# Kernel optimization log

Hardware: AMD Instinct MI355X
Metric: run time of the kernel (lower is better)

The kernel has to match this reference:

```python
import jax, jax.numpy as jnp
import numpy as np

N_NODES = 100000
N_EDGES = 1600000
IN_DIM = 128
HID = 128
OUT = 40


def setup_inputs() -> dict:
    key = jax.random.key(0)
    ks = jax.random.split(key, 8)
    x = jax.random.normal(ks[0], (N_NODES, IN_DIM), dtype=jnp.float32)
    edge_index = jax.random.randint(ks[1], (2, N_EDGES), 0, N_NODES, dtype=jnp.int64)
    def glorot(k, fan_in, fan_out):
        s = jnp.sqrt(6.0 / (fan_in + fan_out)).astype(jnp.float32)
        return jax.random.uniform(k, (fan_in, fan_out), jnp.float32, -s, s)
    return {
        "x": x,
        "edge_index": edge_index,
        "W1": glorot(ks[2], IN_DIM, HID), "b1": jnp.zeros((HID,), jnp.float32),
        "W2": glorot(ks[3], HID, HID),    "b2": jnp.zeros((HID,), jnp.float32),
        "W3": glorot(ks[4], HID, HID),    "b3": jnp.zeros((HID,), jnp.float32),
        "Wl": glorot(ks[5], HID, OUT),    "bl": jnp.zeros((OUT,), jnp.float32),
    }


def _gcn_norm(edge_index, num_nodes):
    # PyG GCNConv default: add self-loops, symmetric normalization.
    loops = jnp.arange(num_nodes, dtype=edge_index.dtype)
    src = jnp.concatenate([edge_index[0], loops])
    dst = jnp.concatenate([edge_index[1], loops])
    deg = jax.ops.segment_sum(jnp.ones_like(dst, dtype=jnp.float32), dst,
                              num_segments=num_nodes)
    dis = jnp.where(deg > 0, jax.lax.rsqrt(deg), 0.0)  # deg^{-1/2}
    norm = dis[src] * dis[dst]  # [E+N]
    return src, dst, norm


def _gcn_conv(x, W, b, src, dst, norm, num_nodes):
    h = x @ W                                   # [N, F_out]
    msg = h[src] * norm[:, None]                # gather + scale
    out = jax.ops.segment_sum(msg, dst, num_segments=num_nodes)
    return out + b


def reference(x, edge_index, W1, b1, W2, b2, W3, b3, Wl, bl):
    n = x.shape[0]
    src, dst, norm = _gcn_norm(edge_index, n)
    h = jax.nn.relu(_gcn_conv(x, W1, b1, src, dst, norm, n))
    h = jax.nn.relu(_gcn_conv(h, W2, b2, src, dst, norm, n))
    h = _gcn_conv(h, W3, b3, src, dst, norm, n)
    # dropout p=0.5 is identity in eval mode
    return h @ Wl + bl
```

## Files before the change

### kernel.cpp

```cpp
#include <hip/hip_runtime.h>

typedef __attribute__((ext_vector_type(8))) short sh8;
typedef __attribute__((ext_vector_type(4))) float f4;

__device__ __forceinline__ float bf2f(unsigned short u) {
    union { unsigned int u; float f; } c; c.u = ((unsigned int)u) << 16; return c.f;
}
__device__ __forceinline__ unsigned short f2bf(float f) {
    union { float f; unsigned int u; } c; c.f = f;
    unsigned int x = c.u;
    unsigned int r = (x + 0x7fffu + ((x >> 16) & 1u)) >> 16;
    return (unsigned short)r;
}
__device__ __forceinline__ void bfsplit(float x, short& hi, short& lo) {
    unsigned short h = f2bf(x);
    float r = x - bf2f(h);
    hi = (short)h;
    lo = (short)f2bf(r);
}

#define CG_BLOCKS 1024
#define CG_COUNT  512
#define CSR_GRID  1568

__global__ void k_init(int* cnt8, int M,
                       const float* __restrict__ W1, unsigned short* __restrict__ sp) {
    int j = blockIdx.x * 256 + threadIdx.x;
    if (j < M) cnt8[j] = 0;
    if (j < 16384) {
        int k = j >> 7, col = j & 127;
        int t = col * 128 + k;
        short h, l;
        bfsplit(W1[j], h, l);
        sp[t] = (unsigned short)h;
        sp[16384 + t] = (unsigned short)l;
    }
}

__device__ __forceinline__ void count_body(const int* __restrict__ dst,
                                           int* __restrict__ cnt8,
                                           int* __restrict__ rank, int E, int N) {
    int cidx = blockIdx.x >> 1;
    int base = (cidx & 7) * N;
    int E4 = E >> 2;
    for (int i = cidx * 256 + threadIdx.x; i < E4; i += CG_COUNT * 256) {
        int4 d = ((const int4*)dst)[i];
        int4 r;
        r.x = ((unsigned)d.x < (unsigned)N) ? atomicAdd(&cnt8[base + d.x], 1) : -1;
        r.y = ((unsigned)d.y < (unsigned)N) ? atomicAdd(&cnt8[base + d.y], 1) : -1;
        r.z = ((unsigned)d.z < (unsigned)N) ? atomicAdd(&cnt8[base + d.z], 1) : -1;
        r.w = ((unsigned)d.w < (unsigned)N) ? atomicAdd(&cnt8[base + d.w], 1) : -1;
        ((int4*)rank)[i] = r;
    }
    if (cidx == 0) {
        for (int e = (E4 << 2) + threadIdx.x; e < E; e += 256) {
            int d = dst[e];
            rank[e] = ((unsigned)d < (unsigned)N) ? atomicAdd(&cnt8[d], 1) : -1;
        }
    }
}

__device__ __forceinline__ void gemm1_body(const float* __restrict__ X,
                                           const unsigned short* __restrict__ Wh,
                                           const unsigned short* __restrict__ Wl,
                                           unsigned short* __restrict__ H, int nPairs) {
    int gidx = blockIdx.x >> 1;
    int wave = threadIdx.x >> 6;
    int lane = threadIdx.x & 63;
    int ln = lane & 15, quad = lane >> 4;
    int c0 = (wave & 1) * 64;
    int subTile = wave >> 1;

    for (int p = gidx; p < nPairs; p += CG_COUNT) {
        int nodeBase = p * 32 + subTile * 16;
        const float* xrow = X + (nodeBase + ln) * 128 + quad * 8;
        sh8 ah[4], al[4];
        #pragma unroll
        for (int kt = 0; kt < 4; ++kt) {
            f4 v0 = *(const f4*)(xrow + kt * 32);
            f4 v1 = *(const f4*)(xrow + kt * 32 + 4);
            #pragma unroll
            for (int j = 0; j < 4; ++j) {
                short h, l;
                bfsplit(v0[j], h, l); ah[kt][j] = h; al[kt][j] = l;
                bfsplit(v1[j], h, l); ah[kt][j + 4] = h; al[kt][j + 4] = l;
            }
        }

        f4 acc[4] = { {0.f,0.f,0.f,0.f}, {0.f,0.f,0.f,0.f}, {0.f,0.f,0.f,0.f}, {0.f,0.f,0.f,0.f} };
        #pragma unroll
        for (int kt = 0; kt < 4; ++kt) {
            int k0 = kt * 32 + quad * 8;
            #pragma unroll
            for (int nt = 0; nt < 4; ++nt) {
                int col = c0 + nt * 16 + ln;
                sh8 bh = *(const sh8*)(Wh + col * 128 + k0);
                sh8 bl = *(const sh8*)(Wl + col * 128 + k0);
                acc[nt] = __builtin_amdgcn_mfma_f32_16x16x32_bf16(ah[kt], bh, acc[nt], 0, 0, 0);
                acc[nt] = __builtin_amdgcn_mfma_f32_16x16x32_bf16(ah[kt], bl, acc[nt], 0, 0, 0);
                acc[nt] = __builtin_amdgcn_mfma_f32_16x16x32_bf16(al[kt], bh, acc[nt], 0, 0, 0);
            }
        }

        #pragma unroll
        for (int nt = 0; nt < 4; ++nt) {
            int col = c0 + nt * 16 + ln;
            #pragma unroll
            for (int r = 0; r < 4; ++r)
                H[(nodeBase + quad * 4 + r) * 128 + col] = f2bf(acc[nt][r]);
        }
    }
}

__global__ __launch_bounds__(256)
void k_count_gemm1(const int* __restrict__ dst, int* __restrict__ cnt8,
                   int* __restrict__ rank, int E, int N,
                   const float* __restrict__ X,
                   const unsigned short* __restrict__ Wh,
                   const unsigned short* __restrict__ Wl,
                   unsigned short* __restrict__ H, int nPairs) {
    if ((blockIdx.x & 1) == 0)
        count_body(dst, cnt8, rank, E, N);
    else
        gemm1_body(X, Wh, Wl, H, nPairs);
}

#define SCAN_B 256
__global__ void k_scan_a(const int* __restrict__ cnt8, int* __restrict__ rowptr,
                         int* __restrict__ off8, int* __restrict__ deg,
                         int* __restrict__ bsum, float* __restrict__ dis, int N) {
    __shared__ int sh[SCAN_B];
    int t = threadIdx.x, i = blockIdx.x * SCAN_B + t;
    int c[8];
    int v = 0;
    if (i < N) {
        #pragma unroll
        for (int g = 0; g < 8; ++g) { c[g] = cnt8[g * N + i]; v += c[g]; }
        dis[i] = rsqrtf((float)(v + 1));
        deg[i] = v;
    }
    sh[t] = v; __syncthreads();
    for (int off = 1; off < SCAN_B; off <<= 1) {
        int x = (t >= off) ? sh[t - off] : 0;
        __syncthreads();
        sh[t] += x;
        __syncthreads();
    }
    int incl = sh[t];
    if (i < N) {
        int b = incl - v;
        rowptr[i] = b;
        int o = b;
        #pragma unroll
        for (int g = 0; g < 8; ++g) { off8[g * N + i] = o; o += c[g]; }
    }
    if (t == SCAN_B - 1) bsum[blockIdx.x] = incl;
}

__global__ void k_scan_b(int* bsum, int NB) {
    __shared__ int sh[512];
    int t = threadIdx.x;
    int v = (t < NB) ? bsum[t] : 0;
    sh[t] = v; __syncthreads();
    for (int off = 1; off < 512; off <<= 1) {
        int x = (t >= off) ? sh[t - off] : 0;
        __syncthreads();
        sh[t] += x;
        __syncthreads();
    }
    if (t < NB) bsum[t] = sh[t] - v;
}

__global__ void k_scan_c(int* __restrict__ rowptr, int* __restrict__ off8,
                         const int* __restrict__ bsum, int N) {
    int i = blockIdx.x * 256 + threadIdx.x;
    if (i < N) {
        int b = bsum[blockIdx.x];
        rowptr[i] += b;
        #pragma unroll
        for (int g = 0; g < 8; ++g) off8[g * N + i] += b;
    }
}

__global__ void k_fill(const int* __restrict__ src, const int* __restrict__ dst,
                       const int* __restrict__ rank, const int* __restrict__ off8,
                       int* __restrict__ csrc, int E, int N) {
    int E4 = E >> 2;
    for (int i = blockIdx.x * 256 + threadIdx.x; i < E4; i += gridDim.x * 256) {
        int g = (i >> 8) & 7;
        const int* off = off8 + g * N;
        int4 d4 = ((const int4*)dst)[i];
        int4 s4 = ((const int4*)src)[i];
        int4 r4 = ((const int4*)rank)[i];
        #pragma unroll
        for (int q = 0; q < 4; ++q) {
            int d = (q == 0) ? d4.x : (q == 1) ? d4.y : (q == 2) ? d4.z : d4.w;
            int s = (q == 0) ? s4.x : (q == 1) ? s4.y : (q == 2) ? s4.z : s4.w;
            int r = (q == 0) ? r4.x : (q == 1) ? r4.y : (q == 2) ? r4.z : r4.w;
            if ((unsigned)d >= (unsigned)N || (unsigned)s >= (unsigned)N || r < 0) continue;
            csrc[off[d] + r] = s;
        }
    }
    if (blockIdx.x == 0) {
        for (int e = (E4 << 2) + threadIdx.x; e < E; e += 256) {
            int d = dst[e];
            int s = src[e];
            int r = rank[e];
            if ((unsigned)d >= (unsigned)N || (unsigned)s >= (unsigned)N || r < 0) continue;
            csrc[off8[d] + r] = s;
        }
    }
}

__global__ __launch_bounds__(256)
void k_gemm128_a16(const unsigned short* __restrict__ X,
                   const float* __restrict__ W,
                   const float* __restrict__ dis,
                   unsigned short* __restrict__ H, int nPairs) {
    int wave = threadIdx.x >> 6;
    int lane = threadIdx.x & 63;
    int ln = lane & 15, quad = lane >> 4;
    int c0 = (wave & 1) * 64;
    int subTile = wave >> 1;

    sh8 bh[4][4], blo[4][4];
    #pragma unroll
    for (int nt = 0; nt < 4; ++nt) {
        int col = c0 + nt * 16 + ln;
        #pragma unroll
        for (int kt = 0; kt < 4; ++kt) {
            int k0 = kt * 32 + quad * 8;
            #pragma unroll
            for (int j = 0; j < 8; ++j) {
                short h, l;
                bfsplit(W[(k0 + j) * 128 + col], h, l);
                bh[nt][kt][j] = h; blo[nt][kt][j] = l;
            }
        }
    }

    int p = blockIdx.x;
    sh8 a[4];
    if (p < nPairs) {
        const unsigned short* xrow = X + ((size_t)(p * 32 + subTile * 16 + ln)) * 128 + quad * 8;
        #pragma unroll
        for (int kt = 0; kt < 4; ++kt) a[kt] = *(const sh8*)(xrow + kt * 32);
    }
    while (p < nPairs) {
        int pn = p + (int)gridDim.x;
        sh8 an[4];
        if (pn < nPairs) {
            const unsigned short* xn = X + ((size_t)(pn * 32 + subTile * 16 + ln)) * 128 + quad * 8;
            #pragma unroll
            for (int kt = 0; kt < 4; ++kt) an[kt] = *(const sh8*)(xn + kt * 32);
        }

        f4 acc[4] = { {0.f,0.f,0.f,0.f}, {0.f,0.f,0.f,0.f}, {0.f,0.f,0.f,0.f}, {0.f,0.f,0.f,0.f} };
        #pragma unroll
        for (int kt = 0; kt < 4; ++kt)
            #pragma unroll
            for (int nt = 0; nt < 4; ++nt) {
                acc[nt] = __builtin_amdgcn_mfma_f32_16x16x32_bf16(a[kt], bh[nt][kt], acc[nt], 0, 0, 0);
                acc[nt] = __builtin_amdgcn_mfma_f32_16x16x32_bf16(a[kt], blo[nt][kt], acc[nt], 0, 0, 0);
            }

        int nodeBase = p * 32 + subTile * 16;
        float ds[4];
        #pragma unroll
        for (int r = 0; r < 4; ++r) ds[r] = dis[nodeBase + quad * 4 + r];
        #pragma unroll
        for (int nt = 0; nt < 4; ++nt) {
            int col = c0 + nt * 16 + ln;
            #pragma unroll
            for (int r = 0; r < 4; ++r)
                H[(nodeBase + quad * 4 + r) * 128 + col] = f2bf(acc[nt][r] * ds[r]);
        }

        #pragma unroll
        for (int kt = 0; kt < 4; ++kt) a[kt] = an[kt];
        p = pn;
    }
}

__global__ __launch_bounds__(256)
void k_agg(const unsigned short* __restrict__ H,
           unsigned short* __restrict__ O,
           const float* __restrict__ dis,
           const int* __restrict__ rowptr,
           const int* __restrict__ deg,
           const int* __restrict__ csrc,
           const float* __restrict__ bias,
           int relu, int scaled, int N) {
    int n = (blockIdx.x * 256 + threadIdx.x) >> 5;
    if (n >= N) return;
    int lane = threadIdx.x & 31;
    int sub  = lane & 15;
    int half = lane >> 4;

    float a0 = 0.f, a1 = 0.f, a2 = 0.f, a3 = 0.f;
    float a4 = 0.f, a5 = 0.f, a6 = 0.f, a7 = 0.f;
    float dn = dis[n];

    auto addrow = [&](uint4 v) {
        a0 += bf2f((unsigned short)v.x);
        a1 += bf2f((unsigned short)(v.x >> 16));
        a2 += bf2f((unsigned short)v.y);
        a3 += bf2f((unsigned short)(v.y >> 16));
        a4 += bf2f((unsigned short)v.z);
        a5 += bf2f((unsigned short)(v.z >> 16));
        a6 += bf2f((unsigned short)v.w);
        a7 += bf2f((unsigned short)(v.w >> 16));
    };
    auto addroww = [&](uint4 v, float w) {
        a0 = fmaf(w, bf2f((unsigned short)v.x), a0);
        a1 = fmaf(w, bf2f((unsigned short)(v.x >> 16)), a1);
        a2 = fmaf(w, bf2f((unsigned short)v.y), a2);
        a3 = fmaf(w, bf2f((unsigned short)(v.y >> 16)), a3);
        a4 = fmaf(w, bf2f((unsigned short)v.z), a4);
        a5 = fmaf(w, bf2f((unsigned short)(v.z >> 16)), a5);
        a6 = fmaf(w, bf2f((unsigned short)v.w), a6);
        a7 = fmaf(w, bf2f((unsigned short)(v.w >> 16)), a7);
    };

    if (half == 0) {
        uint4 v = *(const uint4*)(H + (size_t)n * 128 + sub * 8);
        if (scaled) addrow(v); else addroww(v, dn);
    }

    int start = rowptr[n];
    int e = deg[n];
    int i = 0;
    if (scaled) {
        for (; i + 8 <= e; i += 8) {
            int s[4];
            #pragma unroll
            for (int q = 0; q < 4; ++q) s[q] = csrc[start + i + 2 * q + half];
            uint4 v[4];
            #pragma unroll
            for (int q = 0; q < 4; ++q) v[q] = *(const uint4*)(H + (size_t)s[q] * 128 + sub * 8);
            #pragma unroll
            for (int q = 0; q < 4; ++q) addrow(v[q]);
        }
        for (int j = i + half; j < e; j += 2) {
            int s = csrc[start + j];
            addrow(*(const uint4*)(H + (size_t)s * 128 + sub * 8));
        }
    } else {
        for (; i + 8 <= e; i += 8) {
            int s[4];
            #pragma unroll
            for (int q = 0; q < 4; ++q) s[q] = csrc[start + i + 2 * q + half];
            uint4 v[4];
            #pragma unroll
            for (int q = 0; q < 4; ++q) v[q] = *(const uint4*)(H + (size_t)s[q] * 128 + sub * 8);
            float w[4];
            #pragma unroll
            for (int q = 0; q < 4; ++q) w[q] = dis[s[q]];
            #pragma unroll
            for (int q = 0; q < 4; ++q) addroww(v[q], w[q]);
        }
        for (int j = i + half; j < e; j += 2) {
            int s = csrc[start + j];
            float w = dis[s];
            addroww(*(const uint4*)(H + (size_t)s * 128 + sub * 8), w);
        }
    }

    a0 += __shfl_xor(a0, 16); a1 += __shfl_xor(a1, 16);
    a2 += __shfl_xor(a2, 16); a3 += __shfl_xor(a3, 16);
    a4 += __shfl_xor(a4, 16); a5 += __shfl_xor(a5, 16);
    a6 += __shfl_xor(a6, 16); a7 += __shfl_xor(a7, 16);

    if (half == 0) {
        f4 b0 = *(const f4*)(bias + sub * 8);
        f4 b1 = *(const f4*)(bias + sub * 8 + 4);
        a0 = a0 * dn + b0[0]; a1 = a1 * dn + b0[1];
        a2 = a2 * dn + b0[2]; a3 = a3 * dn + b0[3];
        a4 = a4 * dn + b1[0]; a5 = a5 * dn + b1[1];
        a6 = a6 * dn + b1[2]; a7 = a7 * dn + b1[3];
        if (relu) {
            a0 = fmaxf(a0, 0.f); a1 = fmaxf(a1, 0.f);
            a2 = fmaxf(a2, 0.f); a3 = fmaxf(a3, 0.f);
            a4 = fmaxf(a4, 0.f); a5 = fmaxf(a5, 0.f);
            a6 = fmaxf(a6, 0.f); a7 = fmaxf(a7, 0.f);
        }
        uint4 ov;
        ov.x = (unsigned int)f2bf(a0) | ((unsigned int)f2bf(a1) << 16);
        ov.y = (unsigned int)f2bf(a2) | ((unsigned int)f2bf(a3) << 16);
        ov.z = (unsigned int)f2bf(a4) | ((unsigned int)f2bf(a5) << 16);
        ov.w = (unsigned int)f2bf(a6) | ((unsigned int)f2bf(a7) << 16);
        *(uint4*)(O + (size_t)n * 128 + sub * 8) = ov;
    }
}

__global__ __launch_bounds__(256)
void k_gemm_final(const unsigned short* __restrict__ X,
                  const float* __restrict__ W,
                  const float* __restrict__ bl,
                  float* __restrict__ OUT, int nTiles) {
    int wave = threadIdx.x >> 6;
    int lane = threadIdx.x & 63;
    int ln = lane & 15, quad = lane >> 4;
    int tile = blockIdx.x * 4 + wave;
    if (tile >= nTiles) return;

    sh8 bh[3][4], blo[3][4];
    #pragma unroll
    for (int nt = 0; nt < 3; ++nt) {
        int col = nt * 16 + ln;
        bool valid = (col < 40);
        #pragma unroll
        for (int kt = 0; kt < 4; ++kt) {
            int k0 = kt * 32 + quad * 8;
            #pragma unroll
            for (int j = 0; j < 8; ++j) {
                short h = 0, l = 0;
                if (valid) bfsplit(W[(k0 + j) * 40 + col], h, l);
                bh[nt][kt][j] = h; blo[nt][kt][j] = l;
            }
        }
    }

    int nodeBase = tile * 16;
    const unsigned short* xrow = X + (nodeBase + ln) * 128 + quad * 8;
    sh8 a[4];
    #pragma unroll
    for (int kt = 0; kt < 4; ++kt) a[kt] = *(const sh8*)(xrow + kt * 32);

    f4 acc[3] = { {0.f,0.f,0.f,0.f}, {0.f,0.f,0.f,0.f}, {0.f,0.f,0.f,0.f} };
    #pragma unroll
    for (int kt = 0; kt < 4; ++kt)
        #pragma unroll
        for (int nt = 0; nt < 3; ++nt) {
            acc[nt] = __builtin_amdgcn_mfma_f32_16x16x32_bf16(a[kt], bh[nt][kt], acc[nt], 0, 0, 0);
            acc[nt] = __builtin_amdgcn_mfma_f32_16x16x32_bf16(a[kt], blo[nt][kt], acc[nt], 0, 0, 0);
        }

    #pragma unroll
    for (int nt = 0; nt < 3; ++nt) {
        int col = nt * 16 + ln;
        if (col < 40) {
            float bv = bl[col];
            #pragma unroll
            for (int r = 0; r < 4; ++r)
                OUT[(nodeBase + quad * 4 + r) * 40 + col] = acc[nt][r] + bv;
        }
    }
}

extern "C" void kernel_launch(void* const* d_in, const int* in_sizes, int n_in,
                              void* d_out, int out_size, void* d_ws, size_t ws_size,
                              hipStream_t stream) {
    const float* x  = (const float*)d_in[0];
    const int*   ei = (const int*)d_in[1];
    const float* W1 = (const float*)d_in[2];
    const float* b1 = (const float*)d_in[3];
    const float* W2 = (const float*)d_in[4];
    const float* b2 = (const float*)d_in[5];
    const float* W3 = (const float*)d_in[6];
    const float* b3 = (const float*)d_in[7];
    const float* Wl = (const float*)d_in[8];
    const float* bl = (const float*)d_in[9];

    const int N = in_sizes[0] / 128;
    const int E = in_sizes[1] / 2;
    const int* srcIdx = ei;
    const int* dstIdx = ei + E;

    char* ws = (char*)d_ws;
    size_t off = 0;
    auto alloc = [&](size_t bytes) { void* p = ws + off; off += (bytes + 511) & ~(size_t)511; return p; };
    int*   rowptr  = (int*)  alloc((size_t)N * 4);
    int*   deg     = (int*)  alloc((size_t)N * 4);
    float* dis     = (float*)alloc((size_t)N * 4);
    int*   bsum    = (int*)  alloc(512 * 4);
    unsigned short* wsp = (unsigned short*)alloc(2 * 16384 * 2);
    int*   csrc    = (int*)  alloc((size_t)E * 4);
    unsigned short* h0 = (unsigned short*)alloc((size_t)N * 128 * 2);
    unsigned short* h1 = (unsigned short*)alloc((size_t)N * 128 * 2);
    int* rank = (int*)h1;
    int* off8 = (int*)((char*)h1 + (8u << 20));
    int* cnt8 = (int*)((char*)h1 + (16u << 20));
    unsigned short* Wh1 = wsp;
    unsigned short* Wl1 = wsp + 16384;

    const int gN = (N + 255) / 256;
    const int nPairs = N / 32;
    const int nTiles = N / 16;
    const int gAgg = (N * 32 + 255) / 256;
    const int gZ8 = (N * 8 + 255) / 256;

    k_init<<<gZ8, 256, 0, stream>>>(cnt8, N * 8, W1, wsp);
    k_count_gemm1<<<CG_BLOCKS, 256, 0, stream>>>(dstIdx, cnt8, rank, E, N,
                                                 x, Wh1, Wl1, h0, nPairs);
    k_scan_a<<<gN, 256, 0, stream>>>(cnt8, rowptr, off8, deg, bsum, dis, N);
    k_scan_b<<<1, 512, 0, stream>>>(bsum, gN);
    k_scan_c<<<gN, 256, 0, stream>>>(rowptr, off8, bsum, N);
    k_fill<<<CSR_GRID, 256, 0, stream>>>(srcIdx, dstIdx, rank, off8, csrc, E, N);

    k_agg<<<gAgg, 256, 0, stream>>>(h0, h1, dis, rowptr, deg, csrc, b1, 1, 0, N);
    k_gemm128_a16<<<768, 256, 0, stream>>>(h1, W2, dis, h0, nPairs);
    k_agg<<<gAgg, 256, 0, stream>>>(h0, h1, dis, rowptr, deg, csrc, b2, 1, 1, N);
    k_gemm128_a16<<<768, 256, 0, stream>>>(h1, W3, dis, h0, nPairs);
    k_agg<<<gAgg, 256, 0, stream>>>(h0, h1, dis, rowptr, deg, csrc, b3, 0, 1, N);
    k_gemm_final<<<(nTiles + 3) / 4, 256, 0, stream>>>(h1, Wl, bl, (float*)d_out, nTiles);
}
```

Baseline: 469.8 us.

## Apply final linear before last aggregation to gather narrower 40-column rows

Reassociates the last GCN layer with the output head. The projected features (h·W3) are multiplied by Wl first, stored as bf16 rows padded to 64 columns, and only then aggregated over neighbours. The bias b3·Wl + bl is folded into a 40-entry constant computed in the init kernel. This roughly halves the bytes gathered per edge in the final aggregation and drops the separate 128-wide aggregation pass. In exchange it adds an extra bf16 rounding of the head output before summation, and it writes and reads padding columns that carry no data.

```diff
diff --git a/kernel.cpp b/kernel.cpp
--- a/kernel.cpp
+++ b/kernel.cpp
@@ -24,7 +24,9 @@
 #define CSR_GRID  1568
 
 __global__ void k_init(int* cnt8, int M,
-                       const float* __restrict__ W1, unsigned short* __restrict__ sp) {
+                       const float* __restrict__ W1, unsigned short* __restrict__ sp,
+                       const float* __restrict__ b3, const float* __restrict__ Wl,
+                       const float* __restrict__ bl, float* __restrict__ c40) {
     int j = blockIdx.x * 256 + threadIdx.x;
     if (j < M) cnt8[j] = 0;
     if (j < 16384) {
@@ -34,6 +36,11 @@
         bfsplit(W1[j], h, l);
         sp[t] = (unsigned short)h;
         sp[16384 + t] = (unsigned short)l;
+    }
+    if (j < 40) {
+        float acc = bl[j];
+        for (int k = 0; k < 128; ++k) acc += b3[k] * Wl[k * 40 + j];
+        c40[j] = acc;
     }
 }
 
@@ -394,10 +401,10 @@
 }
 
 __global__ __launch_bounds__(256)
-void k_gemm_final(const unsigned short* __restrict__ X,
-                  const float* __restrict__ W,
-                  const float* __restrict__ bl,
-                  float* __restrict__ OUT, int nTiles) {
+void k_gemm_head(const unsigned short* __restrict__ X,
+                 const float* __restrict__ W,
+                 unsigned short* __restrict__ G,
+                 int nTiles) {
     int wave = threadIdx.x >> 6;
     int lane = threadIdx.x & 63;
     int ln = lane & 15, quad = lane >> 4;
@@ -437,14 +444,84 @@
         }
 
     #pragma unroll
-    for (int nt = 0; nt < 3; ++nt) {
+    for (int nt = 0; nt < 4; ++nt) {
         int col = nt * 16 + ln;
-        if (col < 40) {
-            float bv = bl[col];
-            #pragma unroll
-            for (int r = 0; r < 4; ++r)
-                OUT[(nodeBase + quad * 4 + r) * 40 + col] = acc[nt][r] + bv;
-        }
+        #pragma unroll
+        for (int r = 0; r < 4; ++r) {
+            unsigned short v = 0;
+            if (nt < 3 && col < 40) v = f2bf(acc[nt][r]);
+            G[(size_t)(nodeBase + quad * 4 + r) * 64 + col] = v;
+        }
+    }
+}
+
+__global__ __launch_bounds__(256)
+void k_agg40(const unsigned short* __restrict__ G,
+             float* __restrict__ OUT,
+             const float* __restrict__ dis,
+             const int* __restrict__ rowptr,
+             const int* __restrict__ deg,
+             const int* __restrict__ csrc,
+             const float* __restrict__ c40,
+             int N) {
+    int n = (blockIdx.x * 256 + threadIdx.x) >> 4;
+    if (n >= N) return;
+    int lane = threadIdx.x & 15;
+    int sub  = lane & 7;
+    int half = lane >> 3;
+
+    float a0 = 0.f, a1 = 0.f, a2 = 0.f, a3 = 0.f;
+    float a4 = 0.f, a5 = 0.f, a6 = 0.f, a7 = 0.f;
+
+    auto addrow = [&](uint4 v) {
+        a0 += bf2f((unsigned short)v.x);
+        a1 += bf2f((unsigned short)(v.x >> 16));
+        a2 += bf2f((unsigned short)v.y);
+        a3 += bf2f((unsigned short)(v.y >> 16));
+        a4 += bf2f((unsigned short)v.z);
+        a5 += bf2f((unsigned short)(v.z >> 16));
+        a6 += bf2f((unsigned short)v.w);
+        a7 += bf2f((unsigned short)(v.w >> 16));
+    };
+
+    if (half == 0)
+        addrow(*(const uint4*)(G + (size_t)n * 64 + sub * 8));
+
+    int start = rowptr[n];
+    int e = deg[n];
+    int i = 0;
+    for (; i + 8 <= e; i += 8) {
+        int s[4];
+        #pragma unroll
+        for (int q = 0; q < 4; ++q) s[q] = csrc[start + i + 2 * q + half];
+        uint4 v[4];
+        #pragma unroll
+        for (int q = 0; q < 4; ++q) v[q] = *(const uint4*)(G + (size_t)s[q] * 64 + sub * 8);
+        #pragma unroll
+        for (int q = 0; q < 4; ++q) addrow(v[q]);
+    }
+    for (int j = i + half; j < e; j += 2) {
+        int s = csrc[start + j];
+        addrow(*(const uint4*)(G + (size_t)s * 64 + sub * 8));
+    }
+
+    a0 += __shfl_xor(a0, 8); a1 += __shfl_xor(a1, 8);
+    a2 += __shfl_xor(a2, 8); a3 += __shfl_xor(a3, 8);
+    a4 += __shfl_xor(a4, 8); a5 += __shfl_xor(a5, 8);
+    a6 += __shfl_xor(a6, 8); a7 += __shfl_xor(a7, 8);
+
+    if (half == 0 && sub < 5) {
+        float dn = dis[n];
+        int col0 = sub * 8;
+        const float* c = c40 + col0;
+        f4 o0, o1;
+        o0[0] = a0 * dn + c[0]; o0[1] = a1 * dn + c[1];
+        o0[2] = a2 * dn + c[2]; o0[3] = a3 * dn + c[3];
+        o1[0] = a4 * dn + c[4]; o1[1] = a5 * dn + c[5];
+        o1[2] = a6 * dn + c[6]; o1[3] = a7 * dn + c[7];
+        float* dst = OUT + (size_t)n * 40 + col0;
+        *(f4*)dst = o0;
+        *(f4*)(dst + 4) = o1;
     }
 }
 
@@ -474,6 +551,7 @@
     int*   deg     = (int*)  alloc((size_t)N * 4);
     float* dis     = (float*)alloc((size_t)N * 4);
     int*   bsum    = (int*)  alloc(512 * 4);
+    float* c40     = (float*)alloc(64 * 4);
     unsigned short* wsp = (unsigned short*)alloc(2 * 16384 * 2);
     int*   csrc    = (int*)  alloc((size_t)E * 4);
     unsigned short* h0 = (unsigned short*)alloc((size_t)N * 128 * 2);
@@ -483,14 +561,16 @@
     int* cnt8 = (int*)((char*)h1 + (16u << 20));
     unsigned short* Wh1 = wsp;
     unsigned short* Wl1 = wsp + 16384;
+    unsigned short* g64 = h1;
 
     const int gN = (N + 255) / 256;
     const int nPairs = N / 32;
     const int nTiles = N / 16;
     const int gAgg = (N * 32 + 255) / 256;
+    const int gA40 = (N * 16 + 255) / 256;
     const int gZ8 = (N * 8 + 255) / 256;
 
-    k_init<<<gZ8, 256, 0, stream>>>(cnt8, N * 8, W1, wsp);
+    k_init<<<gZ8, 256, 0, stream>>>(cnt8, N * 8, W1, wsp, b3, Wl, bl, c40);
     k_count_gemm1<<<CG_BLOCKS, 256, 0, stream>>>(dstIdx, cnt8, rank, E, N,
                                                  x, Wh1, Wl1, h0, nPairs);
     k_scan_a<<<gN, 256, 0, stream>>>(cnt8, rowptr, off8, deg, bsum, dis, N);
@@ -502,6 +582,6 @@
     k_gemm128_a16<<<768, 256, 0, stream>>>(h1, W2, dis, h0, nPairs);
     k_agg<<<gAgg, 256, 0, stream>>>(h0, h1, dis, rowptr, deg, csrc, b2, 1, 1, N);
     k_gemm128_a16<<<768, 256, 0, stream>>>(h1, W3, dis, h0, nPairs);
-    k_agg<<<gAgg, 256, 0, stream>>>(h0, h1, dis, rowptr, deg, csrc, b3, 0, 1, N);
-    k_gemm_final<<<(nTiles + 3) / 4, 256, 0, stream>>>(h1, Wl, bl, (float*)d_out, nTiles);
-}
+    k_gemm_head<<<(nTiles + 3) / 4, 256, 0, stream>>>(h0, Wl, g64, nTiles);
+    k_agg40<<<gA40, 256, 0, stream>>>(g64, (float*)d_out, dis, rowptr, deg, csrc, c40, N);
+}
```

New measurement: 448.7 us. -4.5%, faster.
